# Optimization experiments

Measured on AMD Instinct MI355X. Metric: run time of the kernel, lower is better.

## Reference

```python
import jax, jax.numpy as jnp
import numpy as np

H = 14
W_FULL = 14  # spatial width; rfft width = 8


def setup_inputs() -> dict:
    key = jax.random.key(0)
    k1, k2 = jax.random.split(key)
    B, N, C = 256, 196, 768
    x = jax.random.normal(k1, (B, N, C), dtype=jnp.float32)
    complex_weight = jax.random.normal(k2, (14, 8, C, 2), dtype=jnp.float32) * 0.02
    return {"x": x, "complex_weight": complex_weight}


def reference(x, complex_weight):
    B, N, C = x.shape
    Hs = Ws = int(np.sqrt(N))  # 14, static
    xg = x.reshape(B, Hs, Ws, C).astype(jnp.float32)
    # 2D real FFT over spatial dims, orthonormal -> (B, Hs, Ws//2+1, C) complex
    xf = jnp.fft.rfft2(xg, axes=(1, 2), norm="ortho")
    weight = complex_weight[..., 0] + 1j * complex_weight[..., 1]  # (Hs, Ws//2+1, C)
    xf = xf * weight
    out = jnp.fft.irfft2(xf, s=(Hs, Ws), axes=(1, 2), norm="ortho")
    return out.reshape(B, N, C)
```

## Files before the change

kernel.cpp:

```cpp
#include <hip/hip_runtime.h>
#include <hip/hip_bf16.h>


static constexpr int CB     = 64;
static constexpr int NT     = 512;
static constexpr int CTILES = 768 / CB;

typedef float f2 __attribute__((ext_vector_type(2)));

static constexpr float C14[14] = {
     1.0f,
     0.90096886790241915f,  0.62348980185873359f,  0.22252093395631445f,
    -0.22252093395631434f, -0.62348980185873348f, -0.90096886790241915f,
    -1.0f,
    -0.90096886790241926f, -0.62348980185873371f, -0.22252093395631456f,
     0.22252093395631423f,  0.62348980185873337f,  0.90096886790241904f
};
static constexpr float S14[14] = {
     0.0f,
     0.43388373911755812f,  0.78183148246802980f,  0.97492791218182362f,
     0.97492791218182362f,  0.78183148246802991f,  0.43388373911755823f,
     0.0f,
    -0.43388373911755806f, -0.78183148246802958f, -0.97492791218182362f,
    -0.97492791218182373f, -0.78183148246802991f, -0.43388373911755834f
};

__device__ __forceinline__ f2 mk2(float a, float b) { f2 r; r.x = a; r.y = b; return r; }
__device__ __forceinline__ f2 sp2(float a)          { f2 r; r.x = a; r.y = a; return r; }
__device__ __forceinline__ f2 fma2(f2 a, float c, f2 acc) {
    return __builtin_elementwise_fma(a, sp2(c), acc);
}

__device__ __forceinline__ uint32_t pk_bf16(float re, float im) {
    union { __hip_bfloat162 h2; uint32_t u; } cv;
    cv.h2 = __float22bfloat162_rn(make_float2(re, im));
    return cv.u;
}
__device__ __forceinline__ f2 up_bf16(uint32_t v) {
    return mk2(__uint_as_float(v << 16), __uint_as_float(v & 0xffff0000u));
}

__global__ __launch_bounds__(NT, 3) void gfnet_filter(
    const float* __restrict__ x,
    const float* __restrict__ wgt,
    float* __restrict__ out)
{
    __shared__ uint32_t T[14 * 8 * 64];

    const int bid = blockIdx.x;
    const int b   = bid / CTILES;
    const int ct  = bid - b * CTILES;
    const int c0  = ct * CB;
    const int tid = threadIdx.x;
    const int wv  = tid >> 6;
    const int ln  = tid & 63;
    const bool two = (wv < 6);
    const int r0 = wv;
    const int r1 = wv + 8;

    const float* xb = x + (size_t)b * 196 * 768 + c0 + ln;

    f2 Ar[8], Ai[7];
    {
        f2 v[14];
        #pragma unroll
        for (int w = 0; w < 14; ++w) {
            v[w].x = xb[(size_t)(r0 * 14 + w) * 768];
            v[w].y = 0.f;
        }
        if (two) {
            #pragma unroll
            for (int w = 0; w < 14; ++w) v[w].y = xb[(size_t)(r1 * 14 + w) * 768];
        }
        f2 s[7], d[7];
        #pragma unroll
        for (int j = 1; j <= 6; ++j) { s[j] = v[j] + v[14 - j]; d[j] = v[j] - v[14 - j]; }
        const f2 p = v[0] + v[7], q = v[0] - v[7];
        Ar[0] = p + s[1] + s[2] + s[3] + s[4] + s[5] + s[6];
        Ar[7] = q - s[1] + s[2] - s[3] + s[4] - s[5] + s[6];
        #pragma unroll
        for (int u = 1; u <= 6; ++u) {
            f2 re = (u & 1) ? q : p;
            f2 im = sp2(0.f);
            #pragma unroll
            for (int j = 1; j <= 6; ++j) {
                re = fma2(s[j],  C14[(u * j) % 14], re);
                im = fma2(d[j], -S14[(u * j) % 14], im);
            }
            Ar[u] = re; Ai[u] = im;
        }
    }

    #pragma unroll
    for (int u = 0; u < 8; ++u)
        T[(r0 * 8 + u) * 64 + ln] =
            pk_bf16(Ar[u].x, (u >= 1 && u <= 6) ? Ai[u].x : 0.f);
    if (two) {
        #pragma unroll
        for (int u = 0; u < 8; ++u)
            T[(r1 * 8 + u) * 64 + ln] =
                pk_bf16(Ar[u].y, (u >= 1 && u <= 6) ? Ai[u].y : 0.f);
    }

    float wr[14], wi[14];
    {
        const float2* wb = reinterpret_cast<const float2*>(wgt) + (size_t)wv * 768 + c0 + ln;
        #pragma unroll
        for (int k = 0; k < 14; ++k) {
            const float2 t = wb[(size_t)k * (8 * 768)];
            wr[k] = t.x; wi[k] = t.y;
        }
    }

    __syncthreads();

    float gr[14], gi[14];
    #pragma unroll
    for (int h = 0; h < 14; ++h) {
        const f2 t = up_bf16(T[(h * 8 + wv) * 64 + ln]);
        gr[h] = t.x; gi[h] = t.y;
    }

    float esr[3], esi[3], edr[3], edi[3], osr[3], osi[3], odr[3], odi[3];
    #pragma unroll
    for (int i = 0; i < 3; ++i) {
        int j = 2 * (i + 1);
        esr[i] = gr[j] + gr[14 - j]; esi[i] = gi[j] + gi[14 - j];
        edr[i] = gr[j] - gr[14 - j]; edi[i] = gi[j] - gi[14 - j];
        j = 2 * i + 1;
        osr[i] = gr[j] + gr[14 - j]; osi[i] = gi[j] + gi[14 - j];
        odr[i] = gr[j] - gr[14 - j]; odi[i] = gi[j] - gi[14 - j];
    }
    float Ekr[7], Eki[7], Okr[7], Oki[7];
    Ekr[0] = gr[0] + esr[0] + esr[1] + esr[2];
    Eki[0] = gi[0] + esi[0] + esi[1] + esi[2];
    Okr[0] = gr[7] + osr[0] + osr[1] + osr[2];
    Oki[0] = gi[7] + osi[0] + osi[1] + osi[2];
    #pragma unroll
    for (int k = 1; k <= 6; ++k) {
        float er = gr[0], ei = gi[0];
        #pragma unroll
        for (int i = 0; i < 3; ++i) {
            const int j = 2 * (i + 1);
            const float c = C14[(j * k) % 14], s2 = S14[(j * k) % 14];
            er = fmaf(esr[i], c, er); er = fmaf(edi[i],  s2, er);
            ei = fmaf(esi[i], c, ei); ei = fmaf(edr[i], -s2, ei);
        }
        Ekr[k] = er; Eki[k] = ei;
        float onr = (k & 1) ? -gr[7] : gr[7];
        float oni = (k & 1) ? -gi[7] : gi[7];
        #pragma unroll
        for (int i = 0; i < 3; ++i) {
            const int j = 2 * i + 1;
            const float c = C14[(j * k) % 14], s2 = S14[(j * k) % 14];
            onr = fmaf(osr[i], c, onr); onr = fmaf(odi[i],  s2, onr);
            oni = fmaf(osi[i], c, oni); oni = fmaf(odr[i], -s2, oni);
        }
        Okr[k] = onr; Oki[k] = oni;
    }

    float Hr[14], Hi[14];
    #pragma unroll
    for (int k = 0; k < 7; ++k) {
        const float ar = Ekr[k] + Okr[k], ai = Eki[k] + Oki[k];
        const float br = Ekr[k] - Okr[k], bi = Eki[k] - Oki[k];
        Hr[k]     = fmaf(ar, wr[k],     -(ai * wi[k]));
        Hi[k]     = fmaf(ar, wi[k],       ai * wr[k]);
        Hr[k + 7] = fmaf(br, wr[k + 7], -(bi * wi[k + 7]));
        Hi[k + 7] = fmaf(br, wi[k + 7],   bi * wr[k + 7]);
    }

    float qsr[3], qsi[3], qdr[3], qdi[3], rsr[3], rsi[3], rdr[3], rdi[3];
    #pragma unroll
    for (int i = 0; i < 3; ++i) {
        int j = 2 * (i + 1);
        qsr[i] = Hr[j] + Hr[14 - j]; qsi[i] = Hi[j] + Hi[14 - j];
        qdr[i] = Hr[j] - Hr[14 - j]; qdi[i] = Hi[j] - Hi[14 - j];
        j = 2 * i + 1;
        rsr[i] = Hr[j] + Hr[14 - j]; rsi[i] = Hi[j] + Hi[14 - j];
        rdr[i] = Hr[j] - Hr[14 - j]; rdi[i] = Hi[j] - Hi[14 - j];
    }
    float Qr[7], Qi[7], Rr[7], Ri[7];
    Qr[0] = Hr[0] + qsr[0] + qsr[1] + qsr[2];
    Qi[0] = Hi[0] + qsi[0] + qsi[1] + qsi[2];
    Rr[0] = Hr[7] + rsr[0] + rsr[1] + rsr[2];
    Ri[0] = Hi[7] + rsi[0] + rsi[1] + rsi[2];
    #pragma unroll
    for (int m = 1; m <= 6; ++m) {
        float qr = Hr[0], qi2 = Hi[0];
        #pragma unroll
        for (int i = 0; i < 3; ++i) {
            const int j = 2 * (i + 1);
            const float c = C14[(j * m) % 14], s2 = S14[(j * m) % 14];
            qr  = fmaf(qsr[i], c, qr);  qr  = fmaf(qdi[i], -s2, qr);
            qi2 = fmaf(qsi[i], c, qi2); qi2 = fmaf(qdr[i],  s2, qi2);
        }
        Qr[m] = qr; Qi[m] = qi2;
        float rr = (m & 1) ? -Hr[7] : Hr[7];
        float ri2 = (m & 1) ? -Hi[7] : Hi[7];
        #pragma unroll
        for (int i = 0; i < 3; ++i) {
            const int j = 2 * i + 1;
            const float c = C14[(j * m) % 14], s2 = S14[(j * m) % 14];
            rr  = fmaf(rsr[i], c, rr);  rr  = fmaf(rdi[i], -s2, rr);
            ri2 = fmaf(rsi[i], c, ri2); ri2 = fmaf(rdr[i],  s2, ri2);
        }
        Rr[m] = rr; Ri[m] = ri2;
    }

    __syncthreads();

    #pragma unroll
    for (int m = 0; m < 7; ++m) {
        T[(m * 8 + wv) * 64 + ln]       = pk_bf16(Qr[m] + Rr[m], Qi[m] + Ri[m]);
        T[((m + 7) * 8 + wv) * 64 + ln] = pk_bf16(Qr[m] - Rr[m], Qi[m] - Ri[m]);
    }
    __syncthreads();

    float* ob = out + (size_t)b * 196 * 768 + c0 + ln;
    {
        f2 a0[8], b0v[7];
        #pragma unroll
        for (int v = 0; v < 8; ++v) {
            const f2 p0 = up_bf16(T[(r0 * 8 + v) * 64 + ln]);
            f2 p1 = sp2(0.f);
            if (two) p1 = up_bf16(T[(r1 * 8 + v) * 64 + ln]);
            const float beta = (v == 0 || v == 7) ? (1.0f / 196.0f) : (2.0f / 196.0f);
            a0[v] = mk2(p0.x, p1.x) * sp2(beta);
            if (v >= 1 && v <= 6) b0v[v] = mk2(p0.y, p1.y) * sp2(2.0f / 196.0f);
        }
        const f2 pp = a0[0] + a0[7], qq = a0[0] - a0[7];
        const f2 o0 = pp + a0[1] + a0[2] + a0[3] + a0[4] + a0[5] + a0[6];
        const f2 o7 = qq - a0[1] + a0[2] - a0[3] + a0[4] - a0[5] + a0[6];
        __builtin_nontemporal_store(o0.x, &ob[(size_t)(r0 * 14 + 0) * 768]);
        __builtin_nontemporal_store(o7.x, &ob[(size_t)(r0 * 14 + 7) * 768]);
        if (two) {
            __builtin_nontemporal_store(o0.y, &ob[(size_t)(r1 * 14 + 0) * 768]);
            __builtin_nontemporal_store(o7.y, &ob[(size_t)(r1 * 14 + 7) * 768]);
        }
        #pragma unroll
        for (int wp = 1; wp <= 6; ++wp) {
            f2 t1 = (wp & 1) ? qq : pp;
            f2 t2 = sp2(0.f);
            #pragma unroll
            for (int v = 1; v <= 6; ++v) {
                t1 = fma2(a0[v],  C14[(v * wp) % 14], t1);
                t2 = fma2(b0v[v], S14[(v * wp) % 14], t2);
            }
            const f2 om = t1 - t2;
            const f2 op = t1 + t2;
            __builtin_nontemporal_store(om.x, &ob[(size_t)(r0 * 14 + wp) * 768]);
            __builtin_nontemporal_store(op.x, &ob[(size_t)(r0 * 14 + 14 - wp) * 768]);
            if (two) {
                __builtin_nontemporal_store(om.y, &ob[(size_t)(r1 * 14 + wp) * 768]);
                __builtin_nontemporal_store(op.y, &ob[(size_t)(r1 * 14 + 14 - wp) * 768]);
            }
        }
    }
}

extern "C" void kernel_launch(void* const* d_in, const int* in_sizes, int n_in,
                              void* d_out, int out_size, void* d_ws, size_t ws_size,
                              hipStream_t stream) {
    const float* x   = (const float*)d_in[0];
    const float* wgt = (const float*)d_in[1];
    float*       o   = (float*)d_out;

    const int B = in_sizes[0] / (196 * 768);
    dim3 grid(B * CTILES), block(NT);
    gfnet_filter<<<grid, block, 0, stream>>>(x, wgt, o);
}
```

Measured before the change: 56.76 us.

## Process two batches per block with software-pipelined loads and weight reuse

Each block now handles two batch images (b and b+B/2): it loads the second image's input while computing the first, reuses the per-channel filter weights across both, and interleaves the second image's row FFT with the first image's output stores. The grid is halved and launch bounds drop to 2 blocks per SM to leave room for the extra registers. This aims to hide global load latency and cut weight reloads, at the cost of lower occupancy, more register pressure and extra barriers. It assumes B is even.

```diff
diff --git a/kernel.cpp b/kernel.cpp
--- a/kernel.cpp
+++ b/kernel.cpp
@@ -40,16 +40,190 @@
     return mk2(__uint_as_float(v << 16), __uint_as_float(v & 0xffff0000u));
 }
 
-__global__ __launch_bounds__(NT, 3) void gfnet_filter(
+__device__ __forceinline__ void phaseA(const f2 v[14], f2 Ar[8], f2 Ai[7]) {
+    f2 s[7], d[7];
+    #pragma unroll
+    for (int j = 1; j <= 6; ++j) { s[j] = v[j] + v[14 - j]; d[j] = v[j] - v[14 - j]; }
+    const f2 p = v[0] + v[7], q = v[0] - v[7];
+    Ar[0] = p + s[1] + s[2] + s[3] + s[4] + s[5] + s[6];
+    Ar[7] = q - s[1] + s[2] - s[3] + s[4] - s[5] + s[6];
+    #pragma unroll
+    for (int u = 1; u <= 6; ++u) {
+        f2 re = (u & 1) ? q : p;
+        f2 im = sp2(0.f);
+        #pragma unroll
+        for (int j = 1; j <= 6; ++j) {
+            re = fma2(s[j],  C14[(u * j) % 14], re);
+            im = fma2(d[j], -S14[(u * j) % 14], im);
+        }
+        Ar[u] = re; Ai[u] = im;
+    }
+}
+
+__device__ __forceinline__ void gT_write(uint32_t* T, const f2 Ar[8], const f2 Ai[7],
+                                         int r0, int r1, bool two, int ln) {
+    #pragma unroll
+    for (int u = 0; u < 8; ++u)
+        T[(r0 * 8 + u) * 64 + ln] = pk_bf16(Ar[u].x, (u >= 1 && u <= 6) ? Ai[u].x : 0.f);
+    if (two) {
+        #pragma unroll
+        for (int u = 0; u < 8; ++u)
+            T[(r1 * 8 + u) * 64 + ln] = pk_bf16(Ar[u].y, (u >= 1 && u <= 6) ? Ai[u].y : 0.f);
+    }
+}
+
+__device__ __forceinline__ void phaseBWC(const float gr[14], const float gi[14],
+                                         const float wr[14], const float wi[14],
+                                         float Qr[7], float Qi[7], float Rr[7], float Ri[7]) {
+    float esr[3], esi[3], edr[3], edi[3], osr[3], osi[3], odr[3], odi[3];
+    #pragma unroll
+    for (int i = 0; i < 3; ++i) {
+        int j = 2 * (i + 1);
+        esr[i] = gr[j] + gr[14 - j]; esi[i] = gi[j] + gi[14 - j];
+        edr[i] = gr[j] - gr[14 - j]; edi[i] = gi[j] - gi[14 - j];
+        j = 2 * i + 1;
+        osr[i] = gr[j] + gr[14 - j]; osi[i] = gi[j] + gi[14 - j];
+        odr[i] = gr[j] - gr[14 - j]; odi[i] = gi[j] - gi[14 - j];
+    }
+    float Ekr[7], Eki[7], Okr[7], Oki[7];
+    Ekr[0] = gr[0] + esr[0] + esr[1] + esr[2];
+    Eki[0] = gi[0] + esi[0] + esi[1] + esi[2];
+    Okr[0] = gr[7] + osr[0] + osr[1] + osr[2];
+    Oki[0] = gi[7] + osi[0] + osi[1] + osi[2];
+    #pragma unroll
+    for (int k = 1; k <= 6; ++k) {
+        float er = gr[0], ei = gi[0];
+        #pragma unroll
+        for (int i = 0; i < 3; ++i) {
+            const int j = 2 * (i + 1);
+            const float c = C14[(j * k) % 14], s2 = S14[(j * k) % 14];
+            er = fmaf(esr[i], c, er); er = fmaf(edi[i],  s2, er);
+            ei = fmaf(esi[i], c, ei); ei = fmaf(edr[i], -s2, ei);
+        }
+        Ekr[k] = er; Eki[k] = ei;
+        float onr = (k & 1) ? -gr[7] : gr[7];
+        float oni = (k & 1) ? -gi[7] : gi[7];
+        #pragma unroll
+        for (int i = 0; i < 3; ++i) {
+            const int j = 2 * i + 1;
+            const float c = C14[(j * k) % 14], s2 = S14[(j * k) % 14];
+            onr = fmaf(osr[i], c, onr); onr = fmaf(odi[i],  s2, onr);
+            oni = fmaf(osi[i], c, oni); oni = fmaf(odr[i], -s2, oni);
+        }
+        Okr[k] = onr; Oki[k] = oni;
+    }
+    float Hr[14], Hi[14];
+    #pragma unroll
+    for (int k = 0; k < 7; ++k) {
+        const float ar = Ekr[k] + Okr[k], ai = Eki[k] + Oki[k];
+        const float br = Ekr[k] - Okr[k], bi = Eki[k] - Oki[k];
+        Hr[k]     = fmaf(ar, wr[k],     -(ai * wi[k]));
+        Hi[k]     = fmaf(ar, wi[k],       ai * wr[k]);
+        Hr[k + 7] = fmaf(br, wr[k + 7], -(bi * wi[k + 7]));
+        Hi[k + 7] = fmaf(br, wi[k + 7],   bi * wr[k + 7]);
+    }
+    float qsr[3], qsi[3], qdr[3], qdi[3], rsr[3], rsi[3], rdr[3], rdi[3];
+    #pragma unroll
+    for (int i = 0; i < 3; ++i) {
+        int j = 2 * (i + 1);
+        qsr[i] = Hr[j] + Hr[14 - j]; qsi[i] = Hi[j] + Hi[14 - j];
+        qdr[i] = Hr[j] - Hr[14 - j]; qdi[i] = Hi[j] - Hi[14 - j];
+        j = 2 * i + 1;
+        rsr[i] = Hr[j] + Hr[14 - j]; rsi[i] = Hi[j] + Hi[14 - j];
+        rdr[i] = Hr[j] - Hr[14 - j]; rdi[i] = Hi[j] - Hi[14 - j];
+    }
+    Qr[0] = Hr[0] + qsr[0] + qsr[1] + qsr[2];
+    Qi[0] = Hi[0] + qsi[0] + qsi[1] + qsi[2];
+    Rr[0] = Hr[7] + rsr[0] + rsr[1] + rsr[2];
+    Ri[0] = Hi[7] + rsi[0] + rsi[1] + rsi[2];
+    #pragma unroll
+    for (int m = 1; m <= 6; ++m) {
+        float qr = Hr[0], qi2 = Hi[0];
+        #pragma unroll
+        for (int i = 0; i < 3; ++i) {
+            const int j = 2 * (i + 1);
+            const float c = C14[(j * m) % 14], s2 = S14[(j * m) % 14];
+            qr  = fmaf(qsr[i], c, qr);  qr  = fmaf(qdi[i], -s2, qr);
+            qi2 = fmaf(qsi[i], c, qi2); qi2 = fmaf(qdr[i],  s2, qi2);
+        }
+        Qr[m] = qr; Qi[m] = qi2;
+        float rr = (m & 1) ? -Hr[7] : Hr[7];
+        float ri2 = (m & 1) ? -Hi[7] : Hi[7];
+        #pragma unroll
+        for (int i = 0; i < 3; ++i) {
+            const int j = 2 * i + 1;
+            const float c = C14[(j * m) % 14], s2 = S14[(j * m) % 14];
+            rr  = fmaf(rsr[i], c, rr);  rr  = fmaf(rdi[i], -s2, rr);
+            ri2 = fmaf(rsi[i], c, ri2); ri2 = fmaf(rdr[i],  s2, ri2);
+        }
+        Rr[m] = rr; Ri[m] = ri2;
+    }
+}
+
+__device__ __forceinline__ void pT_write(uint32_t* T, const float Qr[7], const float Qi[7],
+                                         const float Rr[7], const float Ri[7], int wv, int ln) {
+    #pragma unroll
+    for (int m = 0; m < 7; ++m) {
+        T[(m * 8 + wv) * 64 + ln]       = pk_bf16(Qr[m] + Rr[m], Qi[m] + Ri[m]);
+        T[((m + 7) * 8 + wv) * 64 + ln] = pk_bf16(Qr[m] - Rr[m], Qi[m] - Ri[m]);
+    }
+}
+
+__device__ __forceinline__ void pRead(const uint32_t* T, f2 a0[8], f2 b0v[7],
+                                      int r0, int r1, bool two, int ln) {
+    #pragma unroll
+    for (int v = 0; v < 8; ++v) {
+        const f2 p0 = up_bf16(T[(r0 * 8 + v) * 64 + ln]);
+        f2 p1 = sp2(0.f);
+        if (two) p1 = up_bf16(T[(r1 * 8 + v) * 64 + ln]);
+        const float beta = (v == 0 || v == 7) ? (1.0f / 196.0f) : (2.0f / 196.0f);
+        a0[v] = mk2(p0.x, p1.x) * sp2(beta);
+        if (v >= 1 && v <= 6) b0v[v] = mk2(p0.y, p1.y) * sp2(2.0f / 196.0f);
+    }
+}
+
+__device__ __forceinline__ void phaseD(const f2 a0[8], const f2 b0v[7], float* ob,
+                                       int r0, int r1, bool two) {
+    const f2 pp = a0[0] + a0[7], qq = a0[0] - a0[7];
+    const f2 o0 = pp + a0[1] + a0[2] + a0[3] + a0[4] + a0[5] + a0[6];
+    const f2 o7 = qq - a0[1] + a0[2] - a0[3] + a0[4] - a0[5] + a0[6];
+    __builtin_nontemporal_store(o0.x, &ob[(size_t)(r0 * 14 + 0) * 768]);
+    __builtin_nontemporal_store(o7.x, &ob[(size_t)(r0 * 14 + 7) * 768]);
+    if (two) {
+        __builtin_nontemporal_store(o0.y, &ob[(size_t)(r1 * 14 + 0) * 768]);
+        __builtin_nontemporal_store(o7.y, &ob[(size_t)(r1 * 14 + 7) * 768]);
+    }
+    #pragma unroll
+    for (int wp = 1; wp <= 6; ++wp) {
+        f2 t1 = (wp & 1) ? qq : pp;
+        f2 t2 = sp2(0.f);
+        #pragma unroll
+        for (int v = 1; v <= 6; ++v) {
+            t1 = fma2(a0[v],  C14[(v * wp) % 14], t1);
+            t2 = fma2(b0v[v], S14[(v * wp) % 14], t2);
+        }
+        const f2 om = t1 - t2;
+        const f2 op = t1 + t2;
+        __builtin_nontemporal_store(om.x, &ob[(size_t)(r0 * 14 + wp) * 768]);
+        __builtin_nontemporal_store(op.x, &ob[(size_t)(r0 * 14 + 14 - wp) * 768]);
+        if (two) {
+            __builtin_nontemporal_store(om.y, &ob[(size_t)(r1 * 14 + wp) * 768]);
+            __builtin_nontemporal_store(op.y, &ob[(size_t)(r1 * 14 + 14 - wp) * 768]);
+        }
+    }
+}
+
+__global__ __launch_bounds__(NT, 2) void gfnet_filter(
     const float* __restrict__ x,
     const float* __restrict__ wgt,
-    float* __restrict__ out)
+    float* __restrict__ out,
+    int bhalf)
 {
     __shared__ uint32_t T[14 * 8 * 64];
 
     const int bid = blockIdx.x;
-    const int b   = bid / CTILES;
-    const int ct  = bid - b * CTILES;
+    const int bb  = bid / CTILES;
+    const int ct  = bid - bb * CTILES;
     const int c0  = ct * CB;
     const int tid = threadIdx.x;
     const int wv  = tid >> 6;
@@ -58,48 +232,21 @@
     const int r0 = wv;
     const int r1 = wv + 8;
 
-    const float* xb = x + (size_t)b * 196 * 768 + c0 + ln;
-
-    f2 Ar[8], Ai[7];
-    {
-        f2 v[14];
-        #pragma unroll
-        for (int w = 0; w < 14; ++w) {
-            v[w].x = xb[(size_t)(r0 * 14 + w) * 768];
-            v[w].y = 0.f;
-        }
-        if (two) {
-            #pragma unroll
-            for (int w = 0; w < 14; ++w) v[w].y = xb[(size_t)(r1 * 14 + w) * 768];
-        }
-        f2 s[7], d[7];
-        #pragma unroll
-        for (int j = 1; j <= 6; ++j) { s[j] = v[j] + v[14 - j]; d[j] = v[j] - v[14 - j]; }
-        const f2 p = v[0] + v[7], q = v[0] - v[7];
-        Ar[0] = p + s[1] + s[2] + s[3] + s[4] + s[5] + s[6];
-        Ar[7] = q - s[1] + s[2] - s[3] + s[4] - s[5] + s[6];
-        #pragma unroll
-        for (int u = 1; u <= 6; ++u) {
-            f2 re = (u & 1) ? q : p;
-            f2 im = sp2(0.f);
-            #pragma unroll
-            for (int j = 1; j <= 6; ++j) {
-                re = fma2(s[j],  C14[(u * j) % 14], re);
-                im = fma2(d[j], -S14[(u * j) % 14], im);
-            }
-            Ar[u] = re; Ai[u] = im;
-        }
-    }
-
-    #pragma unroll
-    for (int u = 0; u < 8; ++u)
-        T[(r0 * 8 + u) * 64 + ln] =
-            pk_bf16(Ar[u].x, (u >= 1 && u <= 6) ? Ai[u].x : 0.f);
+    const size_t toff = (size_t)bhalf * 196 * 768;
+    const float* xb0 = x + (size_t)bb * 196 * 768 + c0 + ln;
+    const float* xb1 = xb0 + toff;
+    float* ob0 = out + (size_t)bb * 196 * 768 + c0 + ln;
+    float* ob1 = ob0 + toff;
+
+    f2 v0[14];
+    #pragma unroll
+    for (int w = 0; w < 14; ++w) {
+        v0[w].x = xb0[(size_t)(r0 * 14 + w) * 768];
+        v0[w].y = 0.f;
+    }
     if (two) {
         #pragma unroll
-        for (int u = 0; u < 8; ++u)
-            T[(r1 * 8 + u) * 64 + ln] =
-                pk_bf16(Ar[u].y, (u >= 1 && u <= 6) ? Ai[u].y : 0.f);
+        for (int w = 0; w < 14; ++w) v0[w].y = xb0[(size_t)(r1 * 14 + w) * 768];
     }
 
     float wr[14], wi[14];
@@ -112,6 +259,21 @@
         }
     }
 
+    f2 Ar[8], Ai[7];
+    phaseA(v0, Ar, Ai);
+    gT_write(T, Ar, Ai, r0, r1, two, ln);
+
+    f2 pv[14];
+    #pragma unroll
+    for (int w = 0; w < 14; ++w) {
+        pv[w].x = xb1[(size_t)(r0 * 14 + w) * 768];
+        pv[w].y = 0.f;
+    }
+    if (two) {
+        #pragma unroll
+        for (int w = 0; w < 14; ++w) pv[w].y = xb1[(size_t)(r1 * 14 + w) * 768];
+    }
+
     __syncthreads();
 
     float gr[14], gi[14];
@@ -120,143 +282,37 @@
         const f2 t = up_bf16(T[(h * 8 + wv) * 64 + ln]);
         gr[h] = t.x; gi[h] = t.y;
     }
-
-    float esr[3], esi[3], edr[3], edi[3], osr[3], osi[3], odr[3], odi[3];
-    #pragma unroll
-    for (int i = 0; i < 3; ++i) {
-        int j = 2 * (i + 1);
-        esr[i] = gr[j] + gr[14 - j]; esi[i] = gi[j] + gi[14 - j];
-        edr[i] = gr[j] - gr[14 - j]; edi[i] = gi[j] - gi[14 - j];
-        j = 2 * i + 1;
-        osr[i] = gr[j] + gr[14 - j]; osi[i] = gi[j] + gi[14 - j];
-        odr[i] = gr[j] - gr[14 - j]; odi[i] = gi[j] - gi[14 - j];
-    }
-    float Ekr[7], Eki[7], Okr[7], Oki[7];
-    Ekr[0] = gr[0] + esr[0] + esr[1] + esr[2];
-    Eki[0] = gi[0] + esi[0] + esi[1] + esi[2];
-    Okr[0] = gr[7] + osr[0] + osr[1] + osr[2];
-    Oki[0] = gi[7] + osi[0] + osi[1] + osi[2];
-    #pragma unroll
-    for (int k = 1; k <= 6; ++k) {
-        float er = gr[0], ei = gi[0];
-        #pragma unroll
-        for (int i = 0; i < 3; ++i) {
-            const int j = 2 * (i + 1);
-            const float c = C14[(j * k) % 14], s2 = S14[(j * k) % 14];
-            er = fmaf(esr[i], c, er); er = fmaf(edi[i],  s2, er);
-            ei = fmaf(esi[i], c, ei); ei = fmaf(edr[i], -s2, ei);
-        }
-        Ekr[k] = er; Eki[k] = ei;
-        float onr = (k & 1) ? -gr[7] : gr[7];
-        float oni = (k & 1) ? -gi[7] : gi[7];
-        #pragma unroll
-        for (int i = 0; i < 3; ++i) {
-            const int j = 2 * i + 1;
-            const float c = C14[(j * k) % 14], s2 = S14[(j * k) % 14];
-            onr = fmaf(osr[i], c, onr); onr = fmaf(odi[i],  s2, onr);
-            oni = fmaf(osi[i], c, oni); oni = fmaf(odr[i], -s2, oni);
-        }
-        Okr[k] = onr; Oki[k] = oni;
-    }
-
-    float Hr[14], Hi[14];
-    #pragma unroll
-    for (int k = 0; k < 7; ++k) {
-        const float ar = Ekr[k] + Okr[k], ai = Eki[k] + Oki[k];
-        const float br = Ekr[k] - Okr[k], bi = Eki[k] - Oki[k];
-        Hr[k]     = fmaf(ar, wr[k],     -(ai * wi[k]));
-        Hi[k]     = fmaf(ar, wi[k],       ai * wr[k]);
-        Hr[k + 7] = fmaf(br, wr[k + 7], -(bi * wi[k + 7]));
-        Hi[k + 7] = fmaf(br, wi[k + 7],   bi * wr[k + 7]);
-    }
-
-    float qsr[3], qsi[3], qdr[3], qdi[3], rsr[3], rsi[3], rdr[3], rdi[3];
-    #pragma unroll
-    for (int i = 0; i < 3; ++i) {
-        int j = 2 * (i + 1);
-        qsr[i] = Hr[j] + Hr[14 - j]; qsi[i] = Hi[j] + Hi[14 - j];
-        qdr[i] = Hr[j] - Hr[14 - j]; qdi[i] = Hi[j] - Hi[14 - j];
-        j = 2 * i + 1;
-        rsr[i] = Hr[j] + Hr[14 - j]; rsi[i] = Hi[j] + Hi[14 - j];
-        rdr[i] = Hr[j] - Hr[14 - j]; rdi[i] = Hi[j] - Hi[14 - j];
-    }
     float Qr[7], Qi[7], Rr[7], Ri[7];
-    Qr[0] = Hr[0] + qsr[0] + qsr[1] + qsr[2];
-    Qi[0] = Hi[0] + qsi[0] + qsi[1] + qsi[2];
-    Rr[0] = Hr[7] + rsr[0] + rsr[1] + rsr[2];
-    Ri[0] = Hi[7] + rsi[0] + rsi[1] + rsi[2];
-    #pragma unroll
-    for (int m = 1; m <= 6; ++m) {
-        float qr = Hr[0], qi2 = Hi[0];
-        #pragma unroll
-        for (int i = 0; i < 3; ++i) {
-            const int j = 2 * (i + 1);
-            const float c = C14[(j * m) % 14], s2 = S14[(j * m) % 14];
-            qr  = fmaf(qsr[i], c, qr);  qr  = fmaf(qdi[i], -s2, qr);
-            qi2 = fmaf(qsi[i], c, qi2); qi2 = fmaf(qdr[i],  s2, qi2);
-        }
-        Qr[m] = qr; Qi[m] = qi2;
-        float rr = (m & 1) ? -Hr[7] : Hr[7];
-        float ri2 = (m & 1) ? -Hi[7] : Hi[7];
-        #pragma unroll
-        for (int i = 0; i < 3; ++i) {
-            const int j = 2 * i + 1;
-            const float c = C14[(j * m) % 14], s2 = S14[(j * m) % 14];
-            rr  = fmaf(rsr[i], c, rr);  rr  = fmaf(rdi[i], -s2, rr);
-            ri2 = fmaf(rsi[i], c, ri2); ri2 = fmaf(rdr[i],  s2, ri2);
-        }
-        Rr[m] = rr; Ri[m] = ri2;
-    }
-
-    __syncthreads();
-
-    #pragma unroll
-    for (int m = 0; m < 7; ++m) {
-        T[(m * 8 + wv) * 64 + ln]       = pk_bf16(Qr[m] + Rr[m], Qi[m] + Ri[m]);
-        T[((m + 7) * 8 + wv) * 64 + ln] = pk_bf16(Qr[m] - Rr[m], Qi[m] - Ri[m]);
-    }
-    __syncthreads();
-
-    float* ob = out + (size_t)b * 196 * 768 + c0 + ln;
-    {
-        f2 a0[8], b0v[7];
-        #pragma unroll
-        for (int v = 0; v < 8; ++v) {
-            const f2 p0 = up_bf16(T[(r0 * 8 + v) * 64 + ln]);
-            f2 p1 = sp2(0.f);
-            if (two) p1 = up_bf16(T[(r1 * 8 + v) * 64 + ln]);
-            const float beta = (v == 0 || v == 7) ? (1.0f / 196.0f) : (2.0f / 196.0f);
-            a0[v] = mk2(p0.x, p1.x) * sp2(beta);
-            if (v >= 1 && v <= 6) b0v[v] = mk2(p0.y, p1.y) * sp2(2.0f / 196.0f);
-        }
-        const f2 pp = a0[0] + a0[7], qq = a0[0] - a0[7];
-        const f2 o0 = pp + a0[1] + a0[2] + a0[3] + a0[4] + a0[5] + a0[6];
-        const f2 o7 = qq - a0[1] + a0[2] - a0[3] + a0[4] - a0[5] + a0[6];
-        __builtin_nontemporal_store(o0.x, &ob[(size_t)(r0 * 14 + 0) * 768]);
-        __builtin_nontemporal_store(o7.x, &ob[(size_t)(r0 * 14 + 7) * 768]);
-        if (two) {
-            __builtin_nontemporal_store(o0.y, &ob[(size_t)(r1 * 14 + 0) * 768]);
-            __builtin_nontemporal_store(o7.y, &ob[(size_t)(r1 * 14 + 7) * 768]);
-        }
-        #pragma unroll
-        for (int wp = 1; wp <= 6; ++wp) {
-            f2 t1 = (wp & 1) ? qq : pp;
-            f2 t2 = sp2(0.f);
-            #pragma unroll
-            for (int v = 1; v <= 6; ++v) {
-                t1 = fma2(a0[v],  C14[(v * wp) % 14], t1);
-                t2 = fma2(b0v[v], S14[(v * wp) % 14], t2);
-            }
-            const f2 om = t1 - t2;
-            const f2 op = t1 + t2;
-            __builtin_nontemporal_store(om.x, &ob[(size_t)(r0 * 14 + wp) * 768]);
-            __builtin_nontemporal_store(op.x, &ob[(size_t)(r0 * 14 + 14 - wp) * 768]);
-            if (two) {
-                __builtin_nontemporal_store(om.y, &ob[(size_t)(r1 * 14 + wp) * 768]);
-                __builtin_nontemporal_store(op.y, &ob[(size_t)(r1 * 14 + 14 - wp) * 768]);
-            }
-        }
-    }
+    phaseBWC(gr, gi, wr, wi, Qr, Qi, Rr, Ri);
+
+    __syncthreads();
+    pT_write(T, Qr, Qi, Rr, Ri, wv, ln);
+    __syncthreads();
+
+    f2 a0[8], b0v[7];
+    pRead(T, a0, b0v, r0, r1, two, ln);
+    __syncthreads();
+
+    phaseA(pv, Ar, Ai);
+    gT_write(T, Ar, Ai, r0, r1, two, ln);
+
+    phaseD(a0, b0v, ob0, r0, r1, two);
+
+    __syncthreads();
+
+    #pragma unroll
+    for (int h = 0; h < 14; ++h) {
+        const f2 t = up_bf16(T[(h * 8 + wv) * 64 + ln]);
+        gr[h] = t.x; gi[h] = t.y;
+    }
+    phaseBWC(gr, gi, wr, wi, Qr, Qi, Rr, Ri);
+
+    __syncthreads();
+    pT_write(T, Qr, Qi, Rr, Ri, wv, ln);
+    __syncthreads();
+
+    pRead(T, a0, b0v, r0, r1, two, ln);
+    phaseD(a0, b0v, ob1, r0, r1, two);
 }
 
 extern "C" void kernel_launch(void* const* d_in, const int* in_sizes, int n_in,
@@ -267,6 +323,7 @@
     float*       o   = (float*)d_out;
 
     const int B = in_sizes[0] / (196 * 768);
-    dim3 grid(B * CTILES), block(NT);
-    gfnet_filter<<<grid, block, 0, stream>>>(x, wgt, o);
-}
+    const int bhalf = B / 2;
+    dim3 grid(bhalf * CTILES), block(NT);
+    gfnet_filter<<<grid, block, 0, stream>>>(x, wgt, o, bhalf);
+}
```

Result: no change. 56.38 us (-0.7%).

## Process two channels per thread with 128-channel tiles and float2 vector I/O

Applied to the files above, without the earlier changes.

Doubles the channel tile to 128 so each thread handles two adjacent channels. Global loads and stores become 8-byte float2 accesses and weight loads become float4, and the arithmetic is packed across the two channels instead of across two spatial rows. The shared staging buffer doubles to uint2 entries and the launch bound drops from 3 to 2 blocks per CU. This halves block count and improves memory access width, at the cost of higher register pressure and lower occupancy.

```diff
diff --git a/kernel.cpp b/kernel.cpp
--- a/kernel.cpp
+++ b/kernel.cpp
@@ -2,7 +2,7 @@
 #include <hip/hip_bf16.h>
 
 
-static constexpr int CB     = 64;
+static constexpr int CB     = 128;
 static constexpr int NT     = 512;
 static constexpr int CTILES = 768 / CB;
 
@@ -30,22 +30,81 @@
 __device__ __forceinline__ f2 fma2(f2 a, float c, f2 acc) {
     return __builtin_elementwise_fma(a, sp2(c), acc);
 }
-
-__device__ __forceinline__ uint32_t pk_bf16(float re, float im) {
+__device__ __forceinline__ f2 fmav(f2 a, f2 b, f2 acc) {
+    return __builtin_elementwise_fma(a, b, acc);
+}
+
+__device__ __forceinline__ uint32_t pk1(float re, float im) {
     union { __hip_bfloat162 h2; uint32_t u; } cv;
     cv.h2 = __float22bfloat162_rn(make_float2(re, im));
     return cv.u;
 }
-__device__ __forceinline__ f2 up_bf16(uint32_t v) {
-    return mk2(__uint_as_float(v << 16), __uint_as_float(v & 0xffff0000u));
-}
-
-__global__ __launch_bounds__(NT, 3) void gfnet_filter(
+__device__ __forceinline__ uint2 pk2(f2 re, f2 im) {
+    uint2 r; r.x = pk1(re.x, im.x); r.y = pk1(re.y, im.y); return r;
+}
+__device__ __forceinline__ f2 up_lo(uint2 v) {
+    return mk2(__uint_as_float(v.x << 16), __uint_as_float(v.y << 16));
+}
+__device__ __forceinline__ f2 up_hi(uint2 v) {
+    return mk2(__uint_as_float(v.x & 0xffff0000u), __uint_as_float(v.y & 0xffff0000u));
+}
+
+__device__ __forceinline__ void phaseA(const f2 v[14], f2 Ar[8], f2 Ai[7]) {
+    f2 s[7], d[7];
+    #pragma unroll
+    for (int j = 1; j <= 6; ++j) { s[j] = v[j] + v[14 - j]; d[j] = v[j] - v[14 - j]; }
+    const f2 p = v[0] + v[7], q = v[0] - v[7];
+    Ar[0] = p + s[1] + s[2] + s[3] + s[4] + s[5] + s[6];
+    Ar[7] = q - s[1] + s[2] - s[3] + s[4] - s[5] + s[6];
+    #pragma unroll
+    for (int u = 1; u <= 6; ++u) {
+        f2 re = (u & 1) ? q : p;
+        f2 im = sp2(0.f);
+        #pragma unroll
+        for (int j = 1; j <= 6; ++j) {
+            re = fma2(s[j],  C14[(u * j) % 14], re);
+            im = fma2(d[j], -S14[(u * j) % 14], im);
+        }
+        Ar[u] = re; Ai[u] = im;
+    }
+}
+
+__device__ __forceinline__ void phaseD_row(const uint2* T2, float* ob, int row, int ln) {
+    f2 a0[8], b0v[7];
+    #pragma unroll
+    for (int v = 0; v < 8; ++v) {
+        const uint2 t = T2[(row * 8 + v) * 64 + ln];
+        const float beta = (v == 0 || v == 7) ? (1.0f / 196.0f) : (2.0f / 196.0f);
+        a0[v] = up_lo(t) * sp2(beta);
+        if (v >= 1 && v <= 6) b0v[v] = up_hi(t) * sp2(2.0f / 196.0f);
+    }
+    const f2 pp = a0[0] + a0[7], qq = a0[0] - a0[7];
+    const f2 o0 = pp + a0[1] + a0[2] + a0[3] + a0[4] + a0[5] + a0[6];
+    const f2 o7 = qq - a0[1] + a0[2] - a0[3] + a0[4] - a0[5] + a0[6];
+    __builtin_nontemporal_store(o0, reinterpret_cast<f2*>(ob + (size_t)(row * 14 + 0) * 768));
+    __builtin_nontemporal_store(o7, reinterpret_cast<f2*>(ob + (size_t)(row * 14 + 7) * 768));
+    #pragma unroll
+    for (int wp = 1; wp <= 6; ++wp) {
+        f2 t1 = (wp & 1) ? qq : pp;
+        f2 t2 = sp2(0.f);
+        #pragma unroll
+        for (int v = 1; v <= 6; ++v) {
+            t1 = fma2(a0[v],  C14[(v * wp) % 14], t1);
+            t2 = fma2(b0v[v], S14[(v * wp) % 14], t2);
+        }
+        __builtin_nontemporal_store(t1 - t2,
+            reinterpret_cast<f2*>(ob + (size_t)(row * 14 + wp) * 768));
+        __builtin_nontemporal_store(t1 + t2,
+            reinterpret_cast<f2*>(ob + (size_t)(row * 14 + 14 - wp) * 768));
+    }
+}
+
+__global__ __launch_bounds__(NT, 2) void gfnet_filter(
     const float* __restrict__ x,
     const float* __restrict__ wgt,
     float* __restrict__ out)
 {
-    __shared__ uint32_t T[14 * 8 * 64];
+    __shared__ uint2 T2[14 * 8 * 64];
 
     const int bid = blockIdx.x;
     const int b   = bid / CTILES;
@@ -58,70 +117,42 @@
     const int r0 = wv;
     const int r1 = wv + 8;
 
-    const float* xb = x + (size_t)b * 196 * 768 + c0 + ln;
-
-    f2 Ar[8], Ai[7];
+    const float* xb = x + (size_t)b * 196 * 768 + c0 + 2 * ln;
+
+    f2 v0[14], v1[14];
+    #pragma unroll
+    for (int w = 0; w < 14; ++w)
+        v0[w] = *reinterpret_cast<const f2*>(xb + (size_t)(r0 * 14 + w) * 768);
+    if (two) {
+        #pragma unroll
+        for (int w = 0; w < 14; ++w)
+            v1[w] = *reinterpret_cast<const f2*>(xb + (size_t)(r1 * 14 + w) * 768);
+    }
+
     {
-        f2 v[14];
-        #pragma unroll
-        for (int w = 0; w < 14; ++w) {
-            v[w].x = xb[(size_t)(r0 * 14 + w) * 768];
-            v[w].y = 0.f;
-        }
+        f2 Ar[8], Ai[7];
+        phaseA(v0, Ar, Ai);
+        #pragma unroll
+        for (int u = 0; u < 8; ++u)
+            T2[(r0 * 8 + u) * 64 + ln] = pk2(Ar[u], (u >= 1 && u <= 6) ? Ai[u] : sp2(0.f));
         if (two) {
+            phaseA(v1, Ar, Ai);
             #pragma unroll
-            for (int w = 0; w < 14; ++w) v[w].y = xb[(size_t)(r1 * 14 + w) * 768];
-        }
-        f2 s[7], d[7];
-        #pragma unroll
-        for (int j = 1; j <= 6; ++j) { s[j] = v[j] + v[14 - j]; d[j] = v[j] - v[14 - j]; }
-        const f2 p = v[0] + v[7], q = v[0] - v[7];
-        Ar[0] = p + s[1] + s[2] + s[3] + s[4] + s[5] + s[6];
-        Ar[7] = q - s[1] + s[2] - s[3] + s[4] - s[5] + s[6];
-        #pragma unroll
-        for (int u = 1; u <= 6; ++u) {
-            f2 re = (u & 1) ? q : p;
-            f2 im = sp2(0.f);
-            #pragma unroll
-            for (int j = 1; j <= 6; ++j) {
-                re = fma2(s[j],  C14[(u * j) % 14], re);
-                im = fma2(d[j], -S14[(u * j) % 14], im);
-            }
-            Ar[u] = re; Ai[u] = im;
-        }
-    }
-
-    #pragma unroll
-    for (int u = 0; u < 8; ++u)
-        T[(r0 * 8 + u) * 64 + ln] =
-            pk_bf16(Ar[u].x, (u >= 1 && u <= 6) ? Ai[u].x : 0.f);
-    if (two) {
-        #pragma unroll
-        for (int u = 0; u < 8; ++u)
-            T[(r1 * 8 + u) * 64 + ln] =
-                pk_bf16(Ar[u].y, (u >= 1 && u <= 6) ? Ai[u].y : 0.f);
-    }
-
-    float wr[14], wi[14];
-    {
-        const float2* wb = reinterpret_cast<const float2*>(wgt) + (size_t)wv * 768 + c0 + ln;
-        #pragma unroll
-        for (int k = 0; k < 14; ++k) {
-            const float2 t = wb[(size_t)k * (8 * 768)];
-            wr[k] = t.x; wi[k] = t.y;
+            for (int u = 0; u < 8; ++u)
+                T2[(r1 * 8 + u) * 64 + ln] = pk2(Ar[u], (u >= 1 && u <= 6) ? Ai[u] : sp2(0.f));
         }
     }
 
     __syncthreads();
 
-    float gr[14], gi[14];
+    f2 gr[14], gi[14];
     #pragma unroll
     for (int h = 0; h < 14; ++h) {
-        const f2 t = up_bf16(T[(h * 8 + wv) * 64 + ln]);
-        gr[h] = t.x; gi[h] = t.y;
-    }
-
-    float esr[3], esi[3], edr[3], edi[3], osr[3], osi[3], odr[3], odi[3];
+        const uint2 t = T2[(h * 8 + wv) * 64 + ln];
+        gr[h] = up_lo(t); gi[h] = up_hi(t);
+    }
+
+    f2 esr[3], esi[3], edr[3], edi[3], osr[3], osi[3], odr[3], odi[3];
     #pragma unroll
     for (int i = 0; i < 3; ++i) {
         int j = 2 * (i + 1);
@@ -131,46 +162,51 @@
         osr[i] = gr[j] + gr[14 - j]; osi[i] = gi[j] + gi[14 - j];
         odr[i] = gr[j] - gr[14 - j]; odi[i] = gi[j] - gi[14 - j];
     }
-    float Ekr[7], Eki[7], Okr[7], Oki[7];
-    Ekr[0] = gr[0] + esr[0] + esr[1] + esr[2];
-    Eki[0] = gi[0] + esi[0] + esi[1] + esi[2];
-    Okr[0] = gr[7] + osr[0] + osr[1] + osr[2];
-    Oki[0] = gi[7] + osi[0] + osi[1] + osi[2];
-    #pragma unroll
-    for (int k = 1; k <= 6; ++k) {
-        float er = gr[0], ei = gi[0];
-        #pragma unroll
-        for (int i = 0; i < 3; ++i) {
-            const int j = 2 * (i + 1);
-            const float c = C14[(j * k) % 14], s2 = S14[(j * k) % 14];
-            er = fmaf(esr[i], c, er); er = fmaf(edi[i],  s2, er);
-            ei = fmaf(esi[i], c, ei); ei = fmaf(edr[i], -s2, ei);
-        }
-        Ekr[k] = er; Eki[k] = ei;
-        float onr = (k & 1) ? -gr[7] : gr[7];
-        float oni = (k & 1) ? -gi[7] : gi[7];
-        #pragma unroll
-        for (int i = 0; i < 3; ++i) {
-            const int j = 2 * i + 1;
-            const float c = C14[(j * k) % 14], s2 = S14[(j * k) % 14];
-            onr = fmaf(osr[i], c, onr); onr = fmaf(odi[i],  s2, onr);
-            oni = fmaf(osi[i], c, oni); oni = fmaf(odr[i], -s2, oni);
-        }
-        Okr[k] = onr; Oki[k] = oni;
-    }
-
-    float Hr[14], Hi[14];
+    const f2 g0r = gr[0], g0i = gi[0], g7r = gr[7], g7i = gi[7];
+
+    const float* wbase = wgt + ((size_t)wv * 768 + c0 + 2 * ln) * 2;
+
+    f2 Hr[14], Hi[14];
     #pragma unroll
     for (int k = 0; k < 7; ++k) {
-        const float ar = Ekr[k] + Okr[k], ai = Eki[k] + Oki[k];
-        const float br = Ekr[k] - Okr[k], bi = Eki[k] - Oki[k];
-        Hr[k]     = fmaf(ar, wr[k],     -(ai * wi[k]));
-        Hi[k]     = fmaf(ar, wi[k],       ai * wr[k]);
-        Hr[k + 7] = fmaf(br, wr[k + 7], -(bi * wi[k + 7]));
-        Hi[k + 7] = fmaf(br, wi[k + 7],   bi * wr[k + 7]);
-    }
-
-    float qsr[3], qsi[3], qdr[3], qdi[3], rsr[3], rsi[3], rdr[3], rdi[3];
+        const float4 wA = *reinterpret_cast<const float4*>(wbase + (size_t)k       * (8 * 768 * 2));
+        const float4 wB = *reinterpret_cast<const float4*>(wbase + (size_t)(k + 7) * (8 * 768 * 2));
+        f2 er, ei, onr, oni;
+        if (k == 0) {
+            er  = g0r + esr[0] + esr[1] + esr[2];
+            ei  = g0i + esi[0] + esi[1] + esi[2];
+            onr = g7r + osr[0] + osr[1] + osr[2];
+            oni = g7i + osi[0] + osi[1] + osi[2];
+        } else {
+            er = g0r; ei = g0i;
+            #pragma unroll
+            for (int i = 0; i < 3; ++i) {
+                const int j = 2 * (i + 1);
+                const float c = C14[(j * k) % 14], s2 = S14[(j * k) % 14];
+                er = fma2(esr[i], c, er); er = fma2(edi[i],  s2, er);
+                ei = fma2(esi[i], c, ei); ei = fma2(edr[i], -s2, ei);
+            }
+            onr = (k & 1) ? -g7r : g7r;
+            oni = (k & 1) ? -g7i : g7i;
+            #pragma unroll
+            for (int i = 0; i < 3; ++i) {
+                const int j = 2 * i + 1;
+                const float c = C14[(j * k) % 14], s2 = S14[(j * k) % 14];
+                onr = fma2(osr[i], c, onr); onr = fma2(odi[i],  s2, onr);
+                oni = fma2(osi[i], c, oni); oni = fma2(odr[i], -s2, oni);
+            }
+        }
+        const f2 ar = er + onr, ai = ei + oni;
+        const f2 br = er - onr, bi = ei - oni;
+        const f2 wAr = mk2(wA.x, wA.z), wAi = mk2(wA.y, wA.w);
+        const f2 wBr = mk2(wB.x, wB.z), wBi = mk2(wB.y, wB.w);
+        Hr[k]     = fmav(ar, wAr, -(ai * wAi));
+        Hi[k]     = fmav(ar, wAi,   ai * wAr);
+        Hr[k + 7] = fmav(br, wBr, -(bi * wBi));
+        Hi[k + 7] = fmav(br, wBi,   bi * wBr);
+    }
+
+    f2 qsr[3], qsi[3], qdr[3], qdi[3], rsr[3], rsi[3], rdr[3], rdi[3];
     #pragma unroll
     for (int i = 0; i < 3; ++i) {
         int j = 2 * (i + 1);
@@ -180,30 +216,30 @@
         rsr[i] = Hr[j] + Hr[14 - j]; rsi[i] = Hi[j] + Hi[14 - j];
         rdr[i] = Hr[j] - Hr[14 - j]; rdi[i] = Hi[j] - Hi[14 - j];
     }
-    float Qr[7], Qi[7], Rr[7], Ri[7];
+    f2 Qr[7], Qi[7], Rr[7], Ri[7];
     Qr[0] = Hr[0] + qsr[0] + qsr[1] + qsr[2];
     Qi[0] = Hi[0] + qsi[0] + qsi[1] + qsi[2];
     Rr[0] = Hr[7] + rsr[0] + rsr[1] + rsr[2];
     Ri[0] = Hi[7] + rsi[0] + rsi[1] + rsi[2];
     #pragma unroll
     for (int m = 1; m <= 6; ++m) {
-        float qr = Hr[0], qi2 = Hi[0];
+        f2 qr = Hr[0], qi2 = Hi[0];
         #pragma unroll
         for (int i = 0; i < 3; ++i) {
             const int j = 2 * (i + 1);
             const float c = C14[(j * m) % 14], s2 = S14[(j * m) % 14];
-            qr  = fmaf(qsr[i], c, qr);  qr  = fmaf(qdi[i], -s2, qr);
-            qi2 = fmaf(qsi[i], c, qi2); qi2 = fmaf(qdr[i],  s2, qi2);
+            qr  = fma2(qsr[i], c, qr);  qr  = fma2(qdi[i], -s2, qr);
+            qi2 = fma2(qsi[i], c, qi2); qi2 = fma2(qdr[i],  s2, qi2);
         }
         Qr[m] = qr; Qi[m] = qi2;
-        float rr = (m & 1) ? -Hr[7] : Hr[7];
-        float ri2 = (m & 1) ? -Hi[7] : Hi[7];
+        f2 rr = (m & 1) ? -Hr[7] : Hr[7];
+        f2 ri2 = (m & 1) ? -Hi[7] : Hi[7];
         #pragma unroll
         for (int i = 0; i < 3; ++i) {
             const int j = 2 * i + 1;
             const float c = C14[(j * m) % 14], s2 = S14[(j * m) % 14];
-            rr  = fmaf(rsr[i], c, rr);  rr  = fmaf(rdi[i], -s2, rr);
-            ri2 = fmaf(rsi[i], c, ri2); ri2 = fmaf(rdr[i],  s2, ri2);
+            rr  = fma2(rsr[i], c, rr);  rr  = fma2(rdi[i], -s2, rr);
+            ri2 = fma2(rsi[i], c, ri2); ri2 = fma2(rdr[i],  s2, ri2);
         }
         Rr[m] = rr; Ri[m] = ri2;
     }
@@ -212,51 +248,14 @@
 
     #pragma unroll
     for (int m = 0; m < 7; ++m) {
-        T[(m * 8 + wv) * 64 + ln]       = pk_bf16(Qr[m] + Rr[m], Qi[m] + Ri[m]);
-        T[((m + 7) * 8 + wv) * 64 + ln] = pk_bf16(Qr[m] - Rr[m], Qi[m] - Ri[m]);
+        T2[(m * 8 + wv) * 64 + ln]       = pk2(Qr[m] + Rr[m], Qi[m] + Ri[m]);
+        T2[((m + 7) * 8 + wv) * 64 + ln] = pk2(Qr[m] - Rr[m], Qi[m] - Ri[m]);
     }
     __syncthreads();
 
-    float* ob = out + (size_t)b * 196 * 768 + c0 + ln;
-    {
-        f2 a0[8], b0v[7];
-        #pragma unroll
-        for (int v = 0; v < 8; ++v) {
-            const f2 p0 = up_bf16(T[(r0 * 8 + v) * 64 + ln]);
-            f2 p1 = sp2(0.f);
-            if (two) p1 = up_bf16(T[(r1 * 8 + v) * 64 + ln]);
-            const float beta = (v == 0 || v == 7) ? (1.0f / 196.0f) : (2.0f / 196.0f);
-            a0[v] = mk2(p0.x, p1.x) * sp2(beta);
-            if (v >= 1 && v <= 6) b0v[v] = mk2(p0.y, p1.y) * sp2(2.0f / 196.0f);
-        }
-        const f2 pp = a0[0] + a0[7], qq = a0[0] - a0[7];
-        const f2 o0 = pp + a0[1] + a0[2] + a0[3] + a0[4] + a0[5] + a0[6];
-        const f2 o7 = qq - a0[1] + a0[2] - a0[3] + a0[4] - a0[5] + a0[6];
-        __builtin_nontemporal_store(o0.x, &ob[(size_t)(r0 * 14 + 0) * 768]);
-        __builtin_nontemporal_store(o7.x, &ob[(size_t)(r0 * 14 + 7) * 768]);
-        if (two) {
-            __builtin_nontemporal_store(o0.y, &ob[(size_t)(r1 * 14 + 0) * 768]);
-            __builtin_nontemporal_store(o7.y, &ob[(size_t)(r1 * 14 + 7) * 768]);
-        }
-        #pragma unroll
-        for (int wp = 1; wp <= 6; ++wp) {
-            f2 t1 = (wp & 1) ? qq : pp;
-            f2 t2 = sp2(0.f);
-            #pragma unroll
-            for (int v = 1; v <= 6; ++v) {
-                t1 = fma2(a0[v],  C14[(v * wp) % 14], t1);
-                t2 = fma2(b0v[v], S14[(v * wp) % 14], t2);
-            }
-            const f2 om = t1 - t2;
-            const f2 op = t1 + t2;
-            __builtin_nontemporal_store(om.x, &ob[(size_t)(r0 * 14 + wp) * 768]);
-            __builtin_nontemporal_store(op.x, &ob[(size_t)(r0 * 14 + 14 - wp) * 768]);
-            if (two) {
-                __builtin_nontemporal_store(om.y, &ob[(size_t)(r1 * 14 + wp) * 768]);
-                __builtin_nontemporal_store(op.y, &ob[(size_t)(r1 * 14 + 14 - wp) * 768]);
-            }
-        }
-    }
+    float* ob = out + (size_t)b * 196 * 768 + c0 + 2 * ln;
+    phaseD_row(T2, ob, r0, ln);
+    if (two) phaseD_row(T2, ob, r1, ln);
 }
 
 extern "C" void kernel_launch(void* const* d_in, const int* in_sizes, int n_in,
```

New measurement: 56.08 us, median of 2. No clear change (-1.2%).
